# Kernel optimization log

Hardware: AMD Instinct MI355X
Metric: run time of the kernel (lower is better)

Reference implementation:

```python
import jax, jax.numpy as jnp
import numpy as np

N = 262144          # number of query points
NUM_AXES = 4        # input_dim + 2
RES = 512           # axis_resolution
EMB = 256           # embedding_dim
OUT = 3             # output_dim
W0 = 30.0           # Sine frequency


def setup_inputs() -> dict:
    key = jax.random.key(0)
    k_c, k_t, k_w1, k_b1, k_w2, k_b2 = jax.random.split(key, 6)
    coords = jax.random.uniform(k_c, (N, 2), jnp.float32, minval=-1.0, maxval=1.0)
    tables = jax.random.normal(k_t, (NUM_AXES, RES, EMB), jnp.float32) * 0.1
    # decoder: Linear(256,256) with first_layer_sine_init, Sine(30), Linear(256,3) with frequency_init(30)
    W1 = jax.random.uniform(k_w1, (256, EMB), jnp.float32, minval=-1.0 / EMB, maxval=1.0 / EMB)
    b1 = jax.random.uniform(k_b1, (256,), jnp.float32, minval=-0.0625, maxval=0.0625)
    lim2 = np.sqrt(6.0 / 256.0) / W0
    W2 = jax.random.uniform(k_w2, (OUT, 256), jnp.float32, minval=-lim2, maxval=lim2)
    b2 = jax.random.uniform(k_b2, (OUT,), jnp.float32, minval=-0.0625, maxval=0.0625)
    return {"coords": coords, "tables": tables, "W1": W1, "b1": b1, "W2": W2, "b2": b2}


def reference(coords, tables, W1, b1, W2, b2):
    # clamp input coords to [-1,1], build the 4 axis coordinates
    c = jnp.clip(coords, -1.0, 1.0)
    c = jnp.concatenate(
        [c, (c[:, 0:1] + c[:, 1:2]) * 0.5, (c[:, 0:1] - c[:, 1:2]) * 0.5], axis=-1
    )  # [N, 4]
    # linearInterpolate (vectorized over all axes at once)
    c = jnp.clip(c, -1.0, 0.999)
    t = (0.5 * c + 0.5) * (tables.shape[1] - 1)       # [N, 4] continuous index
    i0 = jnp.floor(t).astype(jnp.int32)               # [N, 4]
    w = (t - i0)[..., None]                           # [N, 4, 1]
    ax = jnp.arange(tables.shape[0])[None, :]         # [1, 4]
    v0 = tables[ax, i0]                               # [N, 4, EMB] gather
    v1 = tables[ax, i0 + 1]                           # [N, 4, EMB] gather
    emb = jnp.mean((1.0 - w) * v0 + w * v1, axis=1)   # [N, EMB] mean over axes
    # decoder: Linear -> Sine(30) -> Linear
    h = jnp.sin(W0 * (emb @ W1.T + b1))               # [N, 256]
    return h @ W2.T + b2                              # [N, 3]
```

## Files before the change

kernel.cpp:

```cpp
#include <hip/hip_runtime.h>
#include <hip/hip_bf16.h>
#include <hip/hip_fp16.h>

#define NPTS 262144
#define EMB  256
#define RES  512
#define NROWS (4 * RES)

typedef _Float16 half_t;
typedef __attribute__((ext_vector_type(8))) _Float16 half8;
typedef __attribute__((ext_vector_type(2))) _Float16 half2v;

__global__ __launch_bounds__(256) void t2_precompute_kernel(
    const float* __restrict__ tables,
    const float* __restrict__ W1,
    half_t* __restrict__ T2)
{
    __shared__ __align__(16) float arow[8][EMB];
    const int row0 = blockIdx.x * 8;
    const int o = threadIdx.x;

    #pragma unroll
    for (int r = 0; r < 8; ++r)
        arow[r][o] = tables[(row0 + r) * EMB + o];
    __syncthreads();

    float acc[8] = {0.f, 0.f, 0.f, 0.f, 0.f, 0.f, 0.f, 0.f};
    const float4* __restrict__ w1v = reinterpret_cast<const float4*>(W1 + o * EMB);
    for (int ec = 0; ec < EMB / 4; ++ec) {
        const float4 w4 = w1v[ec];
        #pragma unroll
        for (int r = 0; r < 8; ++r) {
            const float4 a4 = *reinterpret_cast<const float4*>(&arow[r][ec * 4]);
            acc[r] = fmaf(w4.x, a4.x, acc[r]);
            acc[r] = fmaf(w4.y, a4.y, acc[r]);
            acc[r] = fmaf(w4.z, a4.z, acc[r]);
            acc[r] = fmaf(w4.w, a4.w, acc[r]);
        }
    }
    const float s = 7.5f * 0.15915494309189535f;
    #pragma unroll
    for (int r = 0; r < 8; ++r)
        T2[(row0 + r) * EMB + o] = (half_t)(s * acc[r]);
}

__global__ __launch_bounds__(256, 4) void eval_kernel(
    const float* __restrict__ coords,
    const half_t* __restrict__ T2,
    const float* __restrict__ b1,
    const float* __restrict__ W2,
    const float* __restrict__ b2,
    float* __restrict__ out)
{
    const int lane = threadIdx.x & 63;
    const int g    = lane >> 4;
    const int l16  = lane & 15;
    const int dA   = l16 * 8;
    const int dB   = 128 + l16 * 8;

    const int wave   = blockIdx.x * 4 + (threadIdx.x >> 6);
    const int nwaves = gridDim.x * 4;

    const float sb = 30.f * 0.15915494309189535f;
    half8 biasA, biasB;
    #pragma unroll
    for (int i = 0; i < 8; ++i) {
        biasA[i] = (half_t)(sb * b1[dA + i]);
        biasB[i] = (half_t)(sb * b1[dB + i]);
    }
    half2v w2p[3][8];
    #pragma unroll
    for (int j = 0; j < 3; ++j)
        #pragma unroll
        for (int k = 0; k < 4; ++k) {
            w2p[j][k][0]     = (half_t)W2[j * EMB + dA + 2 * k];
            w2p[j][k][1]     = (half_t)W2[j * EMB + dA + 2 * k + 1];
            w2p[j][4 + k][0] = (half_t)W2[j * EMB + dB + 2 * k];
            w2p[j][4 + k][1] = (half_t)W2[j * EMB + dB + 2 * k + 1];
        }
    const float ob0 = b2[0], ob1 = b2[1], ob2 = b2[2];
    const char* __restrict__ T2b = reinterpret_cast<const char*>(T2) + (l16 << 4);

    for (int pq = wave; pq < NPTS / 4; pq += nwaves) {
        const int p = 4 * pq + g;
        const float2 cf = *reinterpret_cast<const float2*>(coords + 2 * p);
        const float x = fminf(fmaxf(cf.x, -1.f), 1.f);
        const float y = fminf(fmaxf(cf.y, -1.f), 1.f);

        int rb[4];
        half_t hw[4], homw[4];
        #pragma unroll
        for (int a = 0; a < 4; ++a) {
            float c = (a == 0) ? x : (a == 1) ? y
                    : (a == 2) ? 0.5f * (x + y) : 0.5f * (x - y);
            c = fminf(fmaxf(c, -1.f), 0.999f);
            const float t  = fmaf(c, 255.5f, 255.5f);
            const float fi = floorf(t);
            const float w  = t - fi;
            hw[a]   = (half_t)w;
            homw[a] = (half_t)(1.f - w);
            rb[a]   = (((a << 9) + (int)fi) << 9);
        }

        half8 A0[4], B0[4], A1[4], B1[4];
        #pragma unroll
        for (int a = 0; a < 4; ++a) {
            const char* base = T2b + rb[a];
            A0[a] = *reinterpret_cast<const half8*>(base);
            B0[a] = *reinterpret_cast<const half8*>(base + 256);
            A1[a] = *reinterpret_cast<const half8*>(base + 512);
            B1[a] = *reinterpret_cast<const half8*>(base + 768);
        }

        half8 accA = biasA, accB = biasB;
        #pragma unroll
        for (int a = 0; a < 4; ++a) {
            accA = A0[a] * homw[a] + accA;
            accA = A1[a] * hw[a]   + accA;
            accB = B0[a] * homw[a] + accB;
            accB = B1[a] * hw[a]   + accB;
        }

        float q0 = 0.f, q1 = 0.f, q2 = 0.f;
        #pragma unroll
        for (int k = 0; k < 4; ++k) {
            const float s0 = __builtin_amdgcn_sinf((float)accA[2 * k]);
            const float s1 = __builtin_amdgcn_sinf((float)accA[2 * k + 1]);
#if __has_builtin(__builtin_amdgcn_fdot2)
            const half2v hp = __builtin_bit_cast(half2v, __builtin_amdgcn_cvt_pkrtz(s0, s1));
            q0 = __builtin_amdgcn_fdot2(hp, w2p[0][k], q0, false);
            q1 = __builtin_amdgcn_fdot2(hp, w2p[1][k], q1, false);
            q2 = __builtin_amdgcn_fdot2(hp, w2p[2][k], q2, false);
#else
            q0 = fmaf(s0, (float)w2p[0][k][0], fmaf(s1, (float)w2p[0][k][1], q0));
            q1 = fmaf(s0, (float)w2p[1][k][0], fmaf(s1, (float)w2p[1][k][1], q1));
            q2 = fmaf(s0, (float)w2p[2][k][0], fmaf(s1, (float)w2p[2][k][1], q2));
#endif
        }
        #pragma unroll
        for (int k = 0; k < 4; ++k) {
            const float s0 = __builtin_amdgcn_sinf((float)accB[2 * k]);
            const float s1 = __builtin_amdgcn_sinf((float)accB[2 * k + 1]);
#if __has_builtin(__builtin_amdgcn_fdot2)
            const half2v hp = __builtin_bit_cast(half2v, __builtin_amdgcn_cvt_pkrtz(s0, s1));
            q0 = __builtin_amdgcn_fdot2(hp, w2p[0][4 + k], q0, false);
            q1 = __builtin_amdgcn_fdot2(hp, w2p[1][4 + k], q1, false);
            q2 = __builtin_amdgcn_fdot2(hp, w2p[2][4 + k], q2, false);
#else
            q0 = fmaf(s0, (float)w2p[0][4 + k][0], fmaf(s1, (float)w2p[0][4 + k][1], q0));
            q1 = fmaf(s0, (float)w2p[1][4 + k][0], fmaf(s1, (float)w2p[1][4 + k][1], q1));
            q2 = fmaf(s0, (float)w2p[2][4 + k][0], fmaf(s1, (float)w2p[2][4 + k][1], q2));
#endif
        }

        #pragma unroll
        for (int off = 8; off > 0; off >>= 1) {
            q0 += __shfl_xor(q0, off, 64);
            q1 += __shfl_xor(q1, off, 64);
            q2 += __shfl_xor(q2, off, 64);
        }

        if (l16 == 0) {
            out[3 * p + 0] = q0 + ob0;
            out[3 * p + 1] = q1 + ob1;
            out[3 * p + 2] = q2 + ob2;
        }
    }
}

extern "C" void kernel_launch(void* const* d_in, const int* in_sizes, int n_in,
                              void* d_out, int out_size, void* d_ws, size_t ws_size,
                              hipStream_t stream) {
    const float* coords = (const float*)d_in[0];
    const float* tables = (const float*)d_in[1];
    const float* W1     = (const float*)d_in[2];
    const float* b1     = (const float*)d_in[3];
    const float* W2     = (const float*)d_in[4];
    const float* b2     = (const float*)d_in[5];
    float* out = (float*)d_out;

    half_t* T2 = (half_t*)d_ws;

    hipLaunchKernelGGL(t2_precompute_kernel, dim3(NROWS / 8), dim3(256), 0, stream,
                       tables, W1, T2);
    hipLaunchKernelGGL(eval_kernel, dim3(2048), dim3(256), 0, stream,
                       coords, T2, b1, W2, b2, out);
}
```

Baseline: 59.62 us.

## Sort query points by spatial cell before evaluation to improve gather locality

Adds a counting-sort pipeline (histogram, single-block scan, atomic scatter) that buckets query points into a 128x128 spatial grid, so the eval kernel reads spatially clustered points and its table row gathers hit cache more often. The eval kernel now processes a fixed contiguous chunk per wave with a swizzled block-to-chunk mapping, writes outputs through a permutation index, and uses DPP adds instead of shuffles for the 16-lane reduction. This adds three extra kernels, a memset, global atomics and scattered output writes.

```diff
diff --git a/kernel.cpp b/kernel.cpp
--- a/kernel.cpp
+++ b/kernel.cpp
@@ -6,10 +6,20 @@
 #define EMB  256
 #define RES  512
 #define NROWS (4 * RES)
+#define NCELL (128 * 128)
 
 typedef _Float16 half_t;
 typedef __attribute__((ext_vector_type(8))) _Float16 half8;
 typedef __attribute__((ext_vector_type(2))) _Float16 half2v;
+
+
+__device__ __forceinline__ int cell_of(float x, float y) {
+    const float cx = fminf(fmaxf(x, -1.f), 0.999f);
+    const float cy = fminf(fmaxf(y, -1.f), 0.999f);
+    const int rx = (int)fmaf(cx, 255.5f, 255.5f);
+    const int ry = (int)fmaf(cy, 255.5f, 255.5f);
+    return ((ry >> 2) << 7) | (rx >> 2);
+}
 
 __global__ __launch_bounds__(256) void t2_precompute_kernel(
     const float* __restrict__ tables,
@@ -44,8 +54,65 @@
         T2[(row0 + r) * EMB + o] = (half_t)(s * acc[r]);
 }
 
+__global__ __launch_bounds__(256) void hist_kernel(
+    const float* __restrict__ coords, int* __restrict__ hist)
+{
+    const int p = blockIdx.x * 256 + threadIdx.x;
+    const float x = coords[2 * p], y = coords[2 * p + 1];
+    atomicAdd(&hist[cell_of(x, y)], 1);
+}
+
+__global__ __launch_bounds__(1024) void scan_kernel(
+    const int* __restrict__ hist, int* __restrict__ cursor)
+{
+    __shared__ int ls[1024];
+    const int t = threadIdx.x;
+    int loc[16]; int s = 0;
+    #pragma unroll
+    for (int i = 0; i < 16; ++i) { loc[i] = hist[t * 16 + i]; s += loc[i]; }
+    ls[t] = s;
+    __syncthreads();
+    for (int d = 1; d < 1024; d <<= 1) {
+        int v = 0;
+        if (t >= d) v = ls[t - d];
+        __syncthreads();
+        ls[t] += v;
+        __syncthreads();
+    }
+    int run = ls[t] - s;
+    #pragma unroll
+    for (int i = 0; i < 16; ++i) { cursor[t * 16 + i] = run; run += loc[i]; }
+}
+
+__global__ __launch_bounds__(256) void scatter_kernel(
+    const float* __restrict__ coords, int* __restrict__ cursor,
+    float2* __restrict__ pcoords, int* __restrict__ pidx)
+{
+    const int p = blockIdx.x * 256 + threadIdx.x;
+    const float x = coords[2 * p], y = coords[2 * p + 1];
+    const int idx = atomicAdd(&cursor[cell_of(x, y)], 1);
+    pcoords[idx] = make_float2(fminf(fmaxf(x, -1.f), 1.f),
+                               fminf(fmaxf(y, -1.f), 1.f));
+    pidx[idx] = p;
+}
+
+template <int CTRL>
+__device__ __forceinline__ float dpp_add(float v) {
+    const int vi = __builtin_bit_cast(int, v);
+    const int sh = __builtin_amdgcn_update_dpp(0, vi, CTRL, 0xF, 0xF, true);
+    return v + __builtin_bit_cast(float, sh);
+}
+__device__ __forceinline__ float reduce16(float v) {
+    v = dpp_add<0xB1>(v);
+    v = dpp_add<0x4E>(v);
+    v = dpp_add<0x141>(v);
+    v = dpp_add<0x140>(v);
+    return v;
+}
+
 __global__ __launch_bounds__(256, 4) void eval_kernel(
-    const float* __restrict__ coords,
+    const float2* __restrict__ pcoords,
+    const int* __restrict__ pidx,
     const half_t* __restrict__ T2,
     const float* __restrict__ b1,
     const float* __restrict__ W2,
@@ -58,8 +125,8 @@
     const int dA   = l16 * 8;
     const int dB   = 128 + l16 * 8;
 
-    const int wave   = blockIdx.x * 4 + (threadIdx.x >> 6);
-    const int nwaves = gridDim.x * 4;
+    const int bb   = ((blockIdx.x & 255) << 3) | (blockIdx.x >> 8);
+    const int wave = bb * 4 + (threadIdx.x >> 6);
 
     const float sb = 30.f * 0.15915494309189535f;
     half8 biasA, biasB;
@@ -81,11 +148,12 @@
     const float ob0 = b2[0], ob1 = b2[1], ob2 = b2[2];
     const char* __restrict__ T2b = reinterpret_cast<const char*>(T2) + (l16 << 4);
 
-    for (int pq = wave; pq < NPTS / 4; pq += nwaves) {
-        const int p = 4 * pq + g;
-        const float2 cf = *reinterpret_cast<const float2*>(coords + 2 * p);
-        const float x = fminf(fmaxf(cf.x, -1.f), 1.f);
-        const float y = fminf(fmaxf(cf.y, -1.f), 1.f);
+    const int q0i = wave * 8;
+    for (int q = q0i; q < q0i + 8; ++q) {
+        const int pp = 4 * q + g;
+        const float2 cf = pcoords[pp];
+        const int op = pidx[pp];
+        const float x = cf.x, y = cf.y;
 
         int rb[4];
         half_t hw[4], homw[4];
@@ -153,17 +221,14 @@
 #endif
         }
 
-        #pragma unroll
-        for (int off = 8; off > 0; off >>= 1) {
-            q0 += __shfl_xor(q0, off, 64);
-            q1 += __shfl_xor(q1, off, 64);
-            q2 += __shfl_xor(q2, off, 64);
-        }
+        q0 = reduce16(q0);
+        q1 = reduce16(q1);
+        q2 = reduce16(q2);
 
         if (l16 == 0) {
-            out[3 * p + 0] = q0 + ob0;
-            out[3 * p + 1] = q1 + ob1;
-            out[3 * p + 2] = q2 + ob2;
+            out[3 * op + 0] = q0 + ob0;
+            out[3 * op + 1] = q1 + ob1;
+            out[3 * op + 2] = q2 + ob2;
         }
     }
 }
@@ -179,10 +244,22 @@
     const float* b2     = (const float*)d_in[5];
     float* out = (float*)d_out;
 
-    half_t* T2 = (half_t*)d_ws;
+    char* ws = (char*)d_ws;
+    half_t* T2      = (half_t*)(ws);
+    int*    hist    = (int*)   (ws + (1 << 20));
+    int*    cursor  = (int*)   (ws + (1 << 20) + (1 << 16));
+    float2* pcoords = (float2*)(ws + (1 << 20) + (2 << 16));
+    int*    pidx    = (int*)   (ws + (3 << 20) + (2 << 16));
 
     hipLaunchKernelGGL(t2_precompute_kernel, dim3(NROWS / 8), dim3(256), 0, stream,
                        tables, W1, T2);
+    (void)hipMemsetAsync(hist, 0, NCELL * sizeof(int), stream);
+    hipLaunchKernelGGL(hist_kernel, dim3(NPTS / 256), dim3(256), 0, stream,
+                       coords, hist);
+    hipLaunchKernelGGL(scan_kernel, dim3(1), dim3(1024), 0, stream,
+                       hist, cursor);
+    hipLaunchKernelGGL(scatter_kernel, dim3(NPTS / 256), dim3(256), 0, stream,
+                       coords, cursor, pcoords, pidx);
     hipLaunchKernelGGL(eval_kernel, dim3(2048), dim3(256), 0, stream,
-                       coords, T2, b1, W2, b2, out);
-}
+                       pcoords, pidx, T2, b1, W2, b2, out);
+}
```

Result: slower. 108.9 us (+82.6%).
